# Kernel optimization log

Measured on AMD Instinct MI355X. Metric: run time of the kernel, lower is better.

## Reference

```python
import jax, jax.numpy as jnp
import numpy as np
import math

IN_F = 512
OUT_F = 512
N_EXPERTS = 8
N_GROUPS = 32
TOKENS_PER_GROUP = 2048
N_TOKENS = N_GROUPS * TOKENS_PER_GROUP


def setup_inputs() -> dict:
    key = jax.random.key(0)
    ks = jax.random.split(key, 6)
    k = math.sqrt(1.0 / IN_F)  # init scale from reset_parameters
    x = jax.random.normal(ks[0], (N_TOKENS, IN_F), dtype=jnp.float32)
    # routing coefficients per group (e.g. softmax-like positive weights)
    coefficients = jax.random.uniform(ks[1], (N_GROUPS, N_EXPERTS), dtype=jnp.float32)
    coefficients = coefficients / coefficients.sum(axis=1, keepdims=True)
    weight_experts = jax.random.uniform(ks[2], (N_EXPERTS, OUT_F, IN_F), minval=-k, maxval=k, dtype=jnp.float32)
    bias_experts = jax.random.uniform(ks[3], (N_EXPERTS, OUT_F), minval=-k, maxval=k, dtype=jnp.float32)
    weight_shared = jax.random.uniform(ks[4], (OUT_F, IN_F), minval=-k, maxval=k, dtype=jnp.float32)
    bias_shared = jax.random.uniform(ks[5], (OUT_F,), minval=-k, maxval=k, dtype=jnp.float32)
    sizes = jnp.full((N_GROUPS,), TOKENS_PER_GROUP, dtype=jnp.int32)
    return {
        "x": x,
        "coefficients": coefficients,
        "weight_experts": weight_experts,
        "bias_experts": bias_experts,
        "weight_shared": weight_shared,
        "bias_shared": bias_shared,
        "sizes": sizes,
    }


def reference(x, coefficients, weight_experts, bias_experts, weight_shared, bias_shared, sizes):
    # Routed path: per-group mixed weights  W_g = sum_e coeff[g,e] * W_e  (+ shared)
    G = coefficients.shape[0]
    N = x.shape[0]
    T = N // G  # equal group sizes (static), equivalent to torch.split(x, sizes)
    mixed_w = jnp.einsum('ge,eoi->goi', coefficients, weight_experts) + weight_shared[None]
    mixed_b = jnp.einsum('ge,eo->go', coefficients, bias_experts) + bias_shared[None]
    xg = x.reshape(G, T, -1)                      # [G, T, in]
    out = jnp.einsum('gti,goi->gto', xg, mixed_w) # grouped GEMM, F.linear per group
    out = out + mixed_b[:, None, :]
    return out.reshape(N, -1)
```

## Files before the change

### kernel.cpp

```cpp
#include <hip/hip_runtime.h>
#include <stdint.h>

typedef unsigned short u16;
typedef __attribute__((ext_vector_type(8))) __bf16 bf16x8;
typedef __attribute__((ext_vector_type(4))) __bf16 bf16x4;
typedef __attribute__((ext_vector_type(4))) float f32x4;

#define NGROUPS 32
#define TOK 2048
#define IN_F 512
#define OUT_F 512
#define NEXP 8
#define BM 128
#define BN 128
#define BK 64

__device__ __forceinline__ u16 f2bf(float f) {
    unsigned int u = __float_as_uint(f);
    unsigned int r = (u + 0x7fffu + ((u >> 16) & 1u)) >> 16;
    return (u16)r;
}

__global__ __launch_bounds__(256) void mix_w_kernel(
    const float* __restrict__ coeff, const float* __restrict__ We,
    const float* __restrict__ Wsh, u16* __restrict__ mw)
{
    __shared__ float cs[NGROUPS * NEXP];
    int tid = threadIdx.x;
    cs[tid] = coeff[tid];
    __syncthreads();

    size_t idx = ((size_t)blockIdx.x * 256 + tid) * 4;
    f32x4 wsh = *(const f32x4*)(Wsh + idx);
    f32x4 we[NEXP];
#pragma unroll
    for (int e = 0; e < NEXP; ++e)
        we[e] = *(const f32x4*)(We + (size_t)e * OUT_F * IN_F + idx);

    int g0 = blockIdx.y * 8;
    for (int g = g0; g < g0 + 8; ++g) {
        f32x4 a = wsh;
#pragma unroll
        for (int e = 0; e < NEXP; ++e) {
            float c = cs[g * NEXP + e];
            a[0] += c * we[e][0];
            a[1] += c * we[e][1];
            a[2] += c * we[e][2];
            a[3] += c * we[e][3];
        }
        unsigned int ow[2];
        ow[0] = (unsigned int)f2bf(a[0]) | ((unsigned int)f2bf(a[1]) << 16);
        ow[1] = (unsigned int)f2bf(a[2]) | ((unsigned int)f2bf(a[3]) << 16);
        *(uint2*)(mw + (size_t)g * OUT_F * IN_F + idx) = *(const uint2*)ow;
    }
}

__global__ __launch_bounds__(256) void gemm_kernel(
    const float* __restrict__ x, const u16* __restrict__ mw,
    const float* __restrict__ coeff, const float* __restrict__ be,
    const float* __restrict__ bsh, float* __restrict__ out)
{
    __shared__ __align__(16) u16 As[BM * BK];
    __shared__ __align__(16) u16 Bs[BN * BK];

    int bid = blockIdx.x;
    int xcd = bid & 7;
    int i   = bid >> 3;
    int g = xcd * 4 + (i >> 6);
    int t = i & 63;
    int mtile = t >> 2;
    int ntile = t & 3;

    const float* Ag = x + ((size_t)g * TOK + (size_t)mtile * BM) * IN_F;
    const u16*   Bg = mw + (size_t)g * OUT_F * IN_F + (size_t)ntile * BN * IN_F;

    int tid  = threadIdx.x;
    int lane = tid & 63;
    int wave = tid >> 6;
    int wm = wave >> 1, wn = wave & 1;
    int lm = lane & 15, lq = lane >> 4;

    f32x4 acc[4][4];
#pragma unroll
    for (int mi = 0; mi < 4; ++mi)
#pragma unroll
        for (int ni = 0; ni < 4; ++ni)
            acc[mi][ni] = f32x4{0.f, 0.f, 0.f, 0.f};

    f32x4 areg[8];
#pragma unroll
    for (int j = 0; j < 8; ++j) {
        int L = j * 256 + tid;
        areg[j] = *(const f32x4*)(Ag + (size_t)(L >> 4) * IN_F + (L & 15) * 4);
    }

    for (int kk = 0; kk < IN_F / BK; ++kk) {
        int k0 = kk * BK;
        __syncthreads();

#pragma unroll
        for (int j = 0; j < 8; ++j) {
            int L = j * 256 + tid;
            int r = L >> 4, c4 = L & 15;
            int p = (c4 >> 1) ^ (r & 7);
            bf16x4 bv;
            bv[0] = (__bf16)areg[j][0];
            bv[1] = (__bf16)areg[j][1];
            bv[2] = (__bf16)areg[j][2];
            bv[3] = (__bf16)areg[j][3];
            *(bf16x4*)(As + r * 64 + p * 8 + (c4 & 1) * 4) = bv;
        }
#pragma unroll
        for (int q = 0; q < 4; ++q) {
            int r = q * 32 + (tid >> 3);
            int c = (tid & 7) ^ (r & 7);
            __builtin_amdgcn_global_load_lds(
                (const __attribute__((address_space(1))) void*)(Bg + (size_t)r * IN_F + k0 + c * 8),
                (__attribute__((address_space(3))) void*)(Bs + ((size_t)q * 256 + tid) * 8),
                16, 0, 0);
        }
        __syncthreads();

        if (kk + 1 < IN_F / BK) {
#pragma unroll
            for (int j = 0; j < 8; ++j) {
                int L = j * 256 + tid;
                areg[j] = *(const f32x4*)(Ag + (size_t)(L >> 4) * IN_F + (k0 + BK) + (L & 15) * 4);
            }
        }

#pragma unroll
        for (int ks = 0; ks < 2; ++ks) {
            bf16x8 af[4], bfv[4];
#pragma unroll
            for (int mi = 0; mi < 4; ++mi) {
                int r = wm * 64 + mi * 16 + lm;
                int p = (ks * 4 + lq) ^ (r & 7);
                af[mi] = *(const bf16x8*)(As + r * 64 + p * 8);
            }
#pragma unroll
            for (int ni = 0; ni < 4; ++ni) {
                int r = wn * 64 + ni * 16 + lm;
                int p = (ks * 4 + lq) ^ (r & 7);
                bfv[ni] = *(const bf16x8*)(Bs + r * 64 + p * 8);
            }
#pragma unroll
            for (int mi = 0; mi < 4; ++mi)
#pragma unroll
                for (int ni = 0; ni < 4; ++ni)
                    acc[mi][ni] = __builtin_amdgcn_mfma_f32_16x16x32_bf16(
                        af[mi], bfv[ni], acc[mi][ni], 0, 0, 0);
        }
    }

    int c0 = ntile * BN + wn * 64;
    float cg[NEXP];
#pragma unroll
    for (int e = 0; e < NEXP; ++e) cg[e] = coeff[g * NEXP + e];
    float bias[4];
#pragma unroll
    for (int ni = 0; ni < 4; ++ni) {
        int o = c0 + ni * 16 + lm;
        float v = bsh[o];
#pragma unroll
        for (int e = 0; e < NEXP; ++e) v += cg[e] * be[e * OUT_F + o];
        bias[ni] = v;
    }

    size_t rowbase = (size_t)g * TOK + (size_t)mtile * BM + (size_t)wm * 64;
#pragma unroll
    for (int mi = 0; mi < 4; ++mi) {
#pragma unroll
        for (int rr = 0; rr < 4; ++rr) {
            size_t row = rowbase + mi * 16 + lq * 4 + rr;
            float* orow = out + row * OUT_F;
#pragma unroll
            for (int ni = 0; ni < 4; ++ni)
                orow[c0 + ni * 16 + lm] = acc[mi][ni][rr] + bias[ni];
        }
    }
}

extern "C" void kernel_launch(void* const* d_in, const int* in_sizes, int n_in,
                              void* d_out, int out_size, void* d_ws, size_t ws_size,
                              hipStream_t stream) {
    const float* x     = (const float*)d_in[0];
    const float* coeff = (const float*)d_in[1];
    const float* We    = (const float*)d_in[2];
    const float* be    = (const float*)d_in[3];
    const float* Wsh   = (const float*)d_in[4];
    const float* bsh   = (const float*)d_in[5];
    float* out = (float*)d_out;

    u16* mw = (u16*)d_ws;

    mix_w_kernel<<<dim3(OUT_F * IN_F / (256 * 4), 4), 256, 0, stream>>>(coeff, We, Wsh, mw);

    int grid = NGROUPS * (TOK / BM) * (OUT_F / BN);
    gemm_kernel<<<grid, 256, 0, stream>>>(x, mw, coeff, be, bsh, out);
}
```

Measured before the change: 294.1 us.

## Double-buffer LDS tiles in grouped GEMM to overlap loads with MFMA

```diff
diff --git a/kernel.cpp b/kernel.cpp
--- a/kernel.cpp
+++ b/kernel.cpp
@@ -14,6 +14,7 @@
 #define BM 128
 #define BN 128
 #define BK 64
+#define NKT (IN_F / BK)
 
 __device__ __forceinline__ u16 f2bf(float f) {
     unsigned int u = __float_as_uint(f);
@@ -60,8 +61,8 @@
     const float* __restrict__ coeff, const float* __restrict__ be,
     const float* __restrict__ bsh, float* __restrict__ out)
 {
-    __shared__ __align__(16) u16 As[BM * BK];
-    __shared__ __align__(16) u16 Bs[BN * BK];
+    __shared__ __align__(16) u16 As[2][BM * BK];
+    __shared__ __align__(16) u16 Bs[2][BN * BK];
 
     int bid = blockIdx.x;
     int xcd = bid & 7;
@@ -89,43 +90,54 @@
 
     f32x4 areg[8];
 #pragma unroll
+    for (int q = 0; q < 4; ++q) {
+        int r = q * 32 + (tid >> 3);
+        int c = (tid & 7) ^ (r & 7);
+        __builtin_amdgcn_global_load_lds(
+            (const __attribute__((address_space(1))) void*)(Bg + (size_t)r * IN_F + c * 8),
+            (__attribute__((address_space(3))) void*)(&Bs[0][((size_t)q * 256 + tid) * 8]),
+            16, 0, 0);
+    }
+#pragma unroll
     for (int j = 0; j < 8; ++j) {
         int L = j * 256 + tid;
         areg[j] = *(const f32x4*)(Ag + (size_t)(L >> 4) * IN_F + (L & 15) * 4);
     }
-
-    for (int kk = 0; kk < IN_F / BK; ++kk) {
-        int k0 = kk * BK;
-        __syncthreads();
-
-#pragma unroll
-        for (int j = 0; j < 8; ++j) {
-            int L = j * 256 + tid;
-            int r = L >> 4, c4 = L & 15;
-            int p = (c4 >> 1) ^ (r & 7);
-            bf16x4 bv;
-            bv[0] = (__bf16)areg[j][0];
-            bv[1] = (__bf16)areg[j][1];
-            bv[2] = (__bf16)areg[j][2];
-            bv[3] = (__bf16)areg[j][3];
-            *(bf16x4*)(As + r * 64 + p * 8 + (c4 & 1) * 4) = bv;
-        }
-#pragma unroll
-        for (int q = 0; q < 4; ++q) {
-            int r = q * 32 + (tid >> 3);
-            int c = (tid & 7) ^ (r & 7);
-            __builtin_amdgcn_global_load_lds(
-                (const __attribute__((address_space(1))) void*)(Bg + (size_t)r * IN_F + k0 + c * 8),
-                (__attribute__((address_space(3))) void*)(Bs + ((size_t)q * 256 + tid) * 8),
-                16, 0, 0);
-        }
-        __syncthreads();
-
-        if (kk + 1 < IN_F / BK) {
+#pragma unroll
+    for (int j = 0; j < 8; ++j) {
+        int L = j * 256 + tid;
+        int r = L >> 4, c4 = L & 15;
+        int p = (c4 >> 1) ^ (r & 7);
+        bf16x4 bv;
+        bv[0] = (__bf16)areg[j][0];
+        bv[1] = (__bf16)areg[j][1];
+        bv[2] = (__bf16)areg[j][2];
+        bv[3] = (__bf16)areg[j][3];
+        *(bf16x4*)(&As[0][r * 64 + p * 8 + (c4 & 1) * 4]) = bv;
+    }
+    __syncthreads();
+
+#pragma unroll
+    for (int kk = 0; kk < NKT; ++kk) {
+        const int cur = kk & 1;
+        const int nxt = cur ^ 1;
+        const int k1 = (kk + 1) * BK;
+        const bool more = (kk + 1 < NKT);
+
+        if (more) {
 #pragma unroll
             for (int j = 0; j < 8; ++j) {
                 int L = j * 256 + tid;
-                areg[j] = *(const f32x4*)(Ag + (size_t)(L >> 4) * IN_F + (k0 + BK) + (L & 15) * 4);
+                areg[j] = *(const f32x4*)(Ag + (size_t)(L >> 4) * IN_F + k1 + (L & 15) * 4);
+            }
+#pragma unroll
+            for (int q = 0; q < 4; ++q) {
+                int r = q * 32 + (tid >> 3);
+                int c = (tid & 7) ^ (r & 7);
+                __builtin_amdgcn_global_load_lds(
+                    (const __attribute__((address_space(1))) void*)(Bg + (size_t)r * IN_F + k1 + c * 8),
+                    (__attribute__((address_space(3))) void*)(&Bs[nxt][((size_t)q * 256 + tid) * 8]),
+                    16, 0, 0);
             }
         }
 
@@ -136,13 +148,13 @@
             for (int mi = 0; mi < 4; ++mi) {
                 int r = wm * 64 + mi * 16 + lm;
                 int p = (ks * 4 + lq) ^ (r & 7);
-                af[mi] = *(const bf16x8*)(As + r * 64 + p * 8);
+                af[mi] = *(const bf16x8*)(&As[cur][r * 64 + p * 8]);
             }
 #pragma unroll
             for (int ni = 0; ni < 4; ++ni) {
                 int r = wn * 64 + ni * 16 + lm;
                 int p = (ks * 4 + lq) ^ (r & 7);
-                bfv[ni] = *(const bf16x8*)(Bs + r * 64 + p * 8);
+                bfv[ni] = *(const bf16x8*)(&Bs[cur][r * 64 + p * 8]);
             }
 #pragma unroll
             for (int mi = 0; mi < 4; ++mi)
@@ -150,6 +162,22 @@
                 for (int ni = 0; ni < 4; ++ni)
                     acc[mi][ni] = __builtin_amdgcn_mfma_f32_16x16x32_bf16(
                         af[mi], bfv[ni], acc[mi][ni], 0, 0, 0);
+        }
+
+        if (more) {
+#pragma unroll
+            for (int j = 0; j < 8; ++j) {
+                int L = j * 256 + tid;
+                int r = L >> 4, c4 = L & 15;
+                int p = (c4 >> 1) ^ (r & 7);
+                bf16x4 bv;
+                bv[0] = (__bf16)areg[j][0];
+                bv[1] = (__bf16)areg[j][1];
+                bv[2] = (__bf16)areg[j][2];
+                bv[3] = (__bf16)areg[j][3];
+                *(bf16x4*)(&As[nxt][r * 64 + p * 8 + (c4 & 1) * 4]) = bv;
+            }
+            __syncthreads();
         }
     }
 
```

Result: no change. 295.8 us (+0.6%).
